# Performance work log

Hardware: AMD Instinct MI355X
Metric: run time of the kernel (lower is better)

Reference implementation:

```python
import jax, jax.numpy as jnp
import numpy as np

N_POINTS = 2_000_000
OUTPUT_DIM = 8
L_RES = 128
H_RES = 1024


def _to_idx(c, size):
    # c in [-1, 1], align_corners=True mapping to pixel coords
    p = (c + 1.0) * 0.5 * (size - 1)
    i0 = jnp.floor(p)
    w = p - i0  # interpolation weight toward i1
    i0 = jnp.clip(i0.astype(jnp.int32), 0, size - 1)
    i1 = jnp.clip(i0 + 1, 0, size - 1)
    return i0, i1, w


def trilinear_sample(grid, coords):
    # grid: [C, D, H, W]; coords: [N, 3] with (x->W, y->H, z->D); returns [C, N]
    C, D, H, W = grid.shape
    x0, x1, wx = _to_idx(coords[:, 0], W)
    y0, y1, wy = _to_idx(coords[:, 1], H)
    z0, z1, wz = _to_idx(coords[:, 2], D)
    g = lambda zi, yi, xi: grid[:, zi, yi, xi]  # gather -> [C, N]
    out = (g(z0, y0, x0) * ((1 - wz) * (1 - wy) * (1 - wx))
           + g(z0, y0, x1) * ((1 - wz) * (1 - wy) * wx)
           + g(z0, y1, x0) * ((1 - wz) * wy * (1 - wx))
           + g(z0, y1, x1) * ((1 - wz) * wy * wx)
           + g(z1, y0, x0) * (wz * (1 - wy) * (1 - wx))
           + g(z1, y0, x1) * (wz * (1 - wy) * wx)
           + g(z1, y1, x0) * (wz * wy * (1 - wx))
           + g(z1, y1, x1) * (wz * wy * wx))
    return out


def bilinear_sample(plane, coords):
    # plane: [C, H, W]; coords: [N, 2] with (x->W, y->H); returns [C, N]
    C, H, W = plane.shape
    x0, x1, wx = _to_idx(coords[:, 0], W)
    y0, y1, wy = _to_idx(coords[:, 1], H)
    g = lambda yi, xi: plane[:, yi, xi]  # [C, N]
    out = (g(y0, x0) * ((1 - wy) * (1 - wx))
           + g(y0, x1) * ((1 - wy) * wx)
           + g(y1, x0) * (wy * (1 - wx))
           + g(y1, x1) * (wy * wx))
    return out


def setup_inputs() -> dict:
    key = jax.random.key(0)
    k1, k2, k3 = jax.random.split(key, 3)
    xyz = jax.random.uniform(k1, (N_POINTS, 3), dtype=jnp.float32)  # in [0,1) subset of [-1,1]
    L_grid = jax.random.normal(k2, (1, OUTPUT_DIM, L_RES, L_RES, L_RES), dtype=jnp.float32) * 0.1
    H_planes = jax.random.normal(k3, (3, OUTPUT_DIM, H_RES, H_RES), dtype=jnp.float32) * 0.1
    return {"xyz": xyz, "bound": 1, "L_grid": L_grid, "H_planes": H_planes}


def reference(xyz, bound, L_grid, H_planes):
    xyz_norm = xyz / bound  # [N, 3]
    L_out = trilinear_sample(L_grid[0], xyz_norm)  # [C, N]
    H_out = (bilinear_sample(H_planes[0], xyz_norm[:, jnp.array([0, 1])])
             + bilinear_sample(H_planes[1], xyz_norm[:, jnp.array([1, 2])])
             + bilinear_sample(H_planes[2], xyz_norm[:, jnp.array([2, 0])]))
    return (L_out + H_out).T  # [N, C]
```

## Files before the change

kernel.cpp:

```cpp
#include <hip/hip_runtime.h>

#define LRES 128
#define HRES 1024
#define NB 256
#define BTS 1024
#define NBUCK 512
#define RCAP 8192

static const int LVOX = LRES * LRES * LRES;
static const int PPIX = HRES * HRES;
static const int TV = LVOX + 3 * PPIX;

typedef float f32x4 __attribute__((ext_vector_type(4)));
typedef unsigned u32x4 __attribute__((ext_vector_type(4)));


__device__ __forceinline__ void to_idx(float c, int size, int& i0, int& i1, float& w) {
    float p = (c + 1.0f) * 0.5f * (float)(size - 1);
    float f = floorf(p);
    w = p - f;
    int i = (int)f;
    i0 = min(max(i, 0), size - 1);
    i1 = min(i0 + 1, size - 1);
}

__device__ __forceinline__ unsigned f2bf(float f) {
    unsigned u = __float_as_uint(f);
    return (u + 0x7FFFu + ((u >> 16) & 1u)) >> 16;
}
__device__ __forceinline__ float bflo(unsigned u) { return __uint_as_float(u << 16); }
__device__ __forceinline__ float bfhi(unsigned u) { return __uint_as_float(u & 0xFFFF0000u); }

__device__ __forceinline__ void fma8u(f32x4& a0, f32x4& a1, uint4 q, float w) {
    a0.x = fmaf(bflo(q.x), w, a0.x);
    a0.y = fmaf(bfhi(q.x), w, a0.y);
    a0.z = fmaf(bflo(q.y), w, a0.z);
    a0.w = fmaf(bfhi(q.y), w, a0.w);
    a1.x = fmaf(bflo(q.z), w, a1.x);
    a1.y = fmaf(bfhi(q.z), w, a1.y);
    a1.z = fmaf(bflo(q.w), w, a1.z);
    a1.w = fmaf(bfhi(q.w), w, a1.w);
}

__device__ __forceinline__ unsigned spread3(unsigned x) {
    x &= 0x3FFu;
    x = (x | (x << 16)) & 0x030000FFu;
    x = (x | (x << 8)) & 0x0300F00Fu;
    x = (x | (x << 4)) & 0x030C30C3u;
    x = (x | (x << 2)) & 0x09249249u;
    return x;
}
__device__ __forceinline__ unsigned morton21(float x, float y, float z) {
    int px = min(max((int)(x * 128.f), 0), 127);
    int py = min(max((int)(y * 128.f), 0), 127);
    int pz = min(max((int)(z * 128.f), 0), 127);
    return spread3(px) | (spread3(py) << 1) | (spread3(pz) << 2);
}

__global__ __launch_bounds__(BTS) void prep_k(const float* __restrict__ xyz,
                                              const int* __restrict__ boundp,
                                              const float* __restrict__ Lg,
                                              const float* __restrict__ Hp,
                                              unsigned* __restrict__ hmat,
                                              u32x4* __restrict__ gclb,
                                              u32x4* __restrict__ pclb, int N) {
    __shared__ unsigned h[NBUCK];
    int b = blockIdx.x;
    if (b < NB) {
        for (int i = threadIdx.x; i < NBUCK; i += BTS) h[i] = 0u;
        __syncthreads();
        float invb = 1.0f / (float)boundp[0];
        for (int n = b * BTS + threadIdx.x; n < N; n += NB * BTS) {
            float x = xyz[(size_t)3 * n + 0] * invb;
            float y = xyz[(size_t)3 * n + 1] * invb;
            float z = xyz[(size_t)3 * n + 2] * invb;
            atomicAdd(&h[morton21(x, y, z) >> 12], 1u);
        }
        __syncthreads();
        for (int i = threadIdx.x; i < NBUCK; i += BTS)
            hmat[(size_t)b * NBUCK + i] = h[i];
    } else {
        int v = ((b - NB) * BTS + threadIdx.x) * 2;
        if (v >= TV) return;
        unsigned ha[8], hb[8];
        u32x4* dst;
        if (v < LVOX) {
#pragma unroll
            for (int c = 0; c < 8; ++c) {
                float2 f = *(const float2*)(Lg + (size_t)c * LVOX + v);
                ha[c] = f2bf(f.x);
                hb[c] = f2bf(f.y);
            }
            dst = gclb + v;
        } else {
            int u = v - LVOX;
            int p = u >> 20;
            int r = u & (PPIX - 1);
            const float* src = Hp + (size_t)p * 8 * PPIX;
#pragma unroll
            for (int c = 0; c < 8; ++c) {
                float2 f = *(const float2*)(src + (size_t)c * PPIX + r);
                ha[c] = f2bf(f.x);
                hb[c] = f2bf(f.y);
            }
            dst = pclb + (size_t)p * PPIX + r;
        }
        u32x4 o1, o2;
        o1.x = ha[0] | (ha[1] << 16); o1.y = ha[2] | (ha[3] << 16);
        o1.z = ha[4] | (ha[5] << 16); o1.w = ha[6] | (ha[7] << 16);
        o2.x = hb[0] | (hb[1] << 16); o2.y = hb[2] | (hb[3] << 16);
        o2.z = hb[4] | (hb[5] << 16); o2.w = hb[6] | (hb[7] << 16);
        __builtin_nontemporal_store(o1, dst);
        __builtin_nontemporal_store(o2, dst + 1);
    }
}

__global__ __launch_bounds__(1024) void offsets_k(unsigned* __restrict__ hmat,
                                                  unsigned* __restrict__ bb) {
    __shared__ unsigned tot[NBUCK];
    __shared__ unsigned cbase[NBUCK];
    int t = threadIdx.x;
    unsigned run = 0;
    if (t < NBUCK) {
        for (int b = 0; b < NB; ++b) {
            unsigned v = hmat[(size_t)b * NBUCK + t];
            hmat[(size_t)b * NBUCK + t] = run;
            run += v;
        }
        tot[t] = run;
    }
    __syncthreads();
    for (int o = 1; o < NBUCK; o <<= 1) {
        unsigned v = 0;
        if (t < NBUCK && t >= o) v = tot[t - o];
        __syncthreads();
        if (t < NBUCK) tot[t] += v;
        __syncthreads();
    }
    if (t < NBUCK) {
        unsigned excl = tot[t] - run;
        cbase[t] = excl;
        bb[t] = excl;
        if (t == NBUCK - 1) bb[NBUCK] = tot[t];
    }
    __syncthreads();
    for (int idx = t; idx < NB * NBUCK; idx += 1024)
        hmat[idx] += cbase[idx & (NBUCK - 1)];
}

__global__ __launch_bounds__(BTS) void scatter_k(const float* __restrict__ xyz,
                                                 const int* __restrict__ boundp,
                                                 const unsigned* __restrict__ hmat,
                                                 float4* __restrict__ s1, int N) {
    __shared__ unsigned cnt[NBUCK];
    int b = blockIdx.x;
    for (int i = threadIdx.x; i < NBUCK; i += BTS)
        cnt[i] = hmat[(size_t)b * NBUCK + i];
    __syncthreads();
    float invb = 1.0f / (float)boundp[0];
    for (int n = b * BTS + threadIdx.x; n < N; n += NB * BTS) {
        float x = xyz[(size_t)3 * n + 0] * invb;
        float y = xyz[(size_t)3 * n + 1] * invb;
        float z = xyz[(size_t)3 * n + 2] * invb;
        unsigned key = morton21(x, y, z) >> 12;
        unsigned d = atomicAdd(&cnt[key], 1u);
        s1[d] = make_float4(x, y, z, __int_as_float(n));
    }
}

__global__ __launch_bounds__(1024) void refine_k(const float4* __restrict__ s1,
                                                 const unsigned* __restrict__ bb,
                                                 float4* __restrict__ s2) {
    __shared__ unsigned hist[4096];
    __shared__ unsigned part[1024];
    int b = blockIdx.x;
    unsigned start = bb[b];
    unsigned cnt = bb[b + 1] - start;
    int t = threadIdx.x;
    if (cnt > RCAP) {
        for (unsigned j = t; j < cnt; j += 1024) s2[start + j] = s1[start + j];
        return;
    }
    for (int i = t; i < 4096; i += 1024) hist[i] = 0u;
    __syncthreads();
    float4 rec[RCAP / 1024];
    unsigned key[RCAP / 1024], tick[RCAP / 1024];
#pragma unroll
    for (int k = 0; k < RCAP / 1024; ++k) {
        unsigned j = t + k * 1024u;
        if (j < cnt) {
            rec[k] = s1[start + j];
            key[k] = morton21(rec[k].x, rec[k].y, rec[k].z) & 4095u;
            tick[k] = atomicAdd(&hist[key[k]], 1u);
        }
    }
    __syncthreads();
    unsigned h4[4];
    unsigned s = 0;
#pragma unroll
    for (int k = 0; k < 4; ++k) {
        h4[k] = hist[t * 4 + k];
        s += h4[k];
    }
    part[t] = s;
    __syncthreads();
    for (int o = 1; o < 1024; o <<= 1) {
        unsigned v = (t >= o) ? part[t - o] : 0u;
        __syncthreads();
        part[t] += v;
        __syncthreads();
    }
    unsigned base = part[t] - s;
#pragma unroll
    for (int k = 0; k < 4; ++k) {
        hist[t * 4 + k] = base;
        base += h4[k];
    }
    __syncthreads();
#pragma unroll
    for (int k = 0; k < RCAP / 1024; ++k) {
        unsigned j = t + k * 1024u;
        if (j < cnt) s2[start + hist[key[k]] + tick[k]] = rec[k];
    }
}

__global__ __launch_bounds__(256) void sample_srt(const float4* __restrict__ sorted,
                                                  const uint4* __restrict__ gclb,
                                                  const uint4* __restrict__ pclb,
                                                  float* __restrict__ out, int N) {
    int i = blockIdx.x * blockDim.x + threadIdx.x;
    if (i >= N) return;
    float4 rec = sorted[i];
    float x = rec.x, y = rec.y, z = rec.z;
    int idx = __float_as_int(rec.w);

    int x0, x1, y0, y1, z0, z1;
    float wx, wy, wz;
    to_idx(x, LRES, x0, x1, wx);
    to_idx(y, LRES, y0, y1, wy);
    to_idx(z, LRES, z0, z1, wz);
    const uint4* b00 = gclb + ((size_t)z0 * LRES + y0) * LRES;
    const uint4* b01 = gclb + ((size_t)z0 * LRES + y1) * LRES;
    const uint4* b10 = gclb + ((size_t)z1 * LRES + y0) * LRES;
    const uint4* b11 = gclb + ((size_t)z1 * LRES + y1) * LRES;
    uint4 g0 = b00[x0], g1 = b00[x1], g2 = b01[x0], g3 = b01[x1];
    uint4 g4 = b10[x0], g5 = b10[x1], g6 = b11[x0], g7 = b11[x1];

    const float cw[3] = {x, y, z};
    const float ch[3] = {y, z, x};
    float pww[3], pwh[3];
    uint4 r[12];
#pragma unroll
    for (int p = 0; p < 3; ++p) {
        int w0, w1, h0, h1;
        to_idx(cw[p], HRES, w0, w1, pww[p]);
        to_idx(ch[p], HRES, h0, h1, pwh[p]);
        const uint4* base = pclb + (size_t)p * PPIX;
        const uint4* r0 = base + (size_t)h0 * HRES;
        const uint4* r1 = base + (size_t)h1 * HRES;
        r[4 * p + 0] = r0[w0];
        r[4 * p + 1] = r0[w1];
        r[4 * p + 2] = r1[w0];
        r[4 * p + 3] = r1[w1];
    }

    f32x4 a0 = (f32x4)0.f;
    f32x4 a1 = (f32x4)0.f;
    {
        float ux = 1.f - wx, uy = 1.f - wy, uz = 1.f - wz;
        fma8u(a0, a1, g0, uz * uy * ux);
        fma8u(a0, a1, g1, uz * uy * wx);
        fma8u(a0, a1, g2, uz * wy * ux);
        fma8u(a0, a1, g3, uz * wy * wx);
        fma8u(a0, a1, g4, wz * uy * ux);
        fma8u(a0, a1, g5, wz * uy * wx);
        fma8u(a0, a1, g6, wz * wy * ux);
        fma8u(a0, a1, g7, wz * wy * wx);
    }
#pragma unroll
    for (int p = 0; p < 3; ++p) {
        float ww = pww[p], wh = pwh[p];
        float uw = 1.f - ww, uh = 1.f - wh;
        fma8u(a0, a1, r[4 * p + 0], uh * uw);
        fma8u(a0, a1, r[4 * p + 1], uh * ww);
        fma8u(a0, a1, r[4 * p + 2], wh * uw);
        fma8u(a0, a1, r[4 * p + 3], wh * ww);
    }

    f32x4* o = (f32x4*)(out + (size_t)idx * 8);
    o[0] = a0;
    o[1] = a1;
}

__global__ __launch_bounds__(256) void sample_cf(
    const float* __restrict__ xyz, const int* __restrict__ boundp,
    const float* __restrict__ Lg, const float* __restrict__ Hp,
    float* __restrict__ out, int N) {
    int n = blockIdx.x * blockDim.x + threadIdx.x;
    if (n >= N) return;
    float invb = 1.0f / (float)boundp[0];
    float x = xyz[(size_t)3 * n + 0] * invb;
    float y = xyz[(size_t)3 * n + 1] * invb;
    float z = xyz[(size_t)3 * n + 2] * invb;
    float acc[8];
#pragma unroll
    for (int c = 0; c < 8; ++c) acc[c] = 0.f;
    {
        int x0, x1, y0, y1, z0, z1;
        float wx, wy, wz;
        to_idx(x, LRES, x0, x1, wx);
        to_idx(y, LRES, y0, y1, wy);
        to_idx(z, LRES, z0, z1, wz);
        float ux = 1.f - wx, uy = 1.f - wy, uz = 1.f - wz;
        size_t i8[8];
        i8[0] = ((size_t)z0 * LRES + y0) * LRES + x0;
        i8[1] = ((size_t)z0 * LRES + y0) * LRES + x1;
        i8[2] = ((size_t)z0 * LRES + y1) * LRES + x0;
        i8[3] = ((size_t)z0 * LRES + y1) * LRES + x1;
        i8[4] = ((size_t)z1 * LRES + y0) * LRES + x0;
        i8[5] = ((size_t)z1 * LRES + y0) * LRES + x1;
        i8[6] = ((size_t)z1 * LRES + y1) * LRES + x0;
        i8[7] = ((size_t)z1 * LRES + y1) * LRES + x1;
        float w8[8] = {uz * uy * ux, uz * uy * wx, uz * wy * ux, uz * wy * wx,
                       wz * uy * ux, wz * uy * wx, wz * wy * ux, wz * wy * wx};
#pragma unroll
        for (int c = 0; c < 8; ++c) {
            const float* g = Lg + (size_t)c * LVOX;
            float s = 0.f;
#pragma unroll
            for (int k = 0; k < 8; ++k) s = fmaf(g[i8[k]], w8[k], s);
            acc[c] += s;
        }
    }
    {
        const float cw[3] = {x, y, z};
        const float ch[3] = {y, z, x};
        for (int p = 0; p < 3; ++p) {
            int w0, w1, h0, h1;
            float ww, wh;
            to_idx(cw[p], HRES, w0, w1, ww);
            to_idx(ch[p], HRES, h0, h1, wh);
            float uw = 1.f - ww, uh = 1.f - wh;
            size_t i4[4] = {(size_t)h0 * HRES + w0, (size_t)h0 * HRES + w1,
                            (size_t)h1 * HRES + w0, (size_t)h1 * HRES + w1};
            float w4[4] = {uh * uw, uh * ww, wh * uw, wh * ww};
            const float* pb = Hp + (size_t)p * 8 * PPIX;
#pragma unroll
            for (int c = 0; c < 8; ++c) {
                const float* g = pb + (size_t)c * PPIX;
                float s = 0.f;
#pragma unroll
                for (int k = 0; k < 4; ++k) s = fmaf(g[i4[k]], w4[k], s);
                acc[c] += s;
            }
        }
    }
#pragma unroll
    for (int c = 0; c < 8; ++c) out[(size_t)n * 8 + c] = acc[c];
}

extern "C" void kernel_launch(void* const* d_in, const int* in_sizes, int n_in,
                              void* d_out, int out_size, void* d_ws, size_t ws_size,
                              hipStream_t stream) {
    const float* xyz = (const float*)d_in[0];
    const int* bound = (const int*)d_in[1];
    const float* Lg = (const float*)d_in[2];
    const float* Hp = (const float*)d_in[3];
    float* out = (float*)d_out;
    int N = in_sizes[0] / 3;

    size_t off = 0;
    size_t gclb_b = (size_t)LVOX * 16;
    size_t pclb_b = (size_t)3 * PPIX * 16;
    size_t s1_b = (size_t)N * 16;
    size_t s2_b = (size_t)N * 16;
    size_t hmat_b = (size_t)NB * NBUCK * 4;
    size_t bb_b = (size_t)(NBUCK + 1) * 4;
    size_t need = gclb_b + pclb_b + s1_b + s2_b + hmat_b + bb_b;

    if (ws_size >= need) {
        char* w = (char*)d_ws;
        u32x4* gclb = (u32x4*)(w + off);       off += gclb_b;
        u32x4* pclb = (u32x4*)(w + off);       off += pclb_b;
        float4* s1 = (float4*)(w + off);       off += s1_b;
        float4* s2 = (float4*)(w + off);       off += s2_b;
        unsigned* hmat = (unsigned*)(w + off); off += hmat_b;
        unsigned* bb = (unsigned*)(w + off);

        int prep_blocks = NB + (TV / 2 + BTS - 1) / BTS;
        prep_k<<<prep_blocks, BTS, 0, stream>>>(xyz, bound, Lg, Hp, hmat, gclb, pclb, N);
        offsets_k<<<1, 1024, 0, stream>>>(hmat, bb);
        scatter_k<<<NB, BTS, 0, stream>>>(xyz, bound, hmat, s1, N);
        refine_k<<<NBUCK, 1024, 0, stream>>>(s1, bb, s2);
        sample_srt<<<(N + 255) / 256, 256, 0, stream>>>(s2, (const uint4*)gclb,
                                                        (const uint4*)pclb, out, N);
    } else {
        sample_cf<<<(N + 255) / 256, 256, 0, stream>>>(xyz, bound, Lg, Hp, out, N);
    }
}
```

Measured before the change: 408.3 us.

## Vectorize xyz loads, widen grid conversion, and transpose histogram matrix layout

The histogram and scatter kernels now read xyz as three 16-byte vectors covering four points per thread, instead of three scalar loads per point. The bf16 grid conversion handles four voxels per thread with 16-byte nontemporal loads, halving the number of conversion blocks. The per-block histogram matrix is transposed to bucket-major order, so the prefix-scan thread for each bucket walks a contiguous row with vector loads and the base-offset pass is vectorized. The aim is fewer memory transactions in the preprocessing kernels. In exchange each thread holds more registers, and the scatter order inside a bucket changes.

Measured after the change: 497.7 us. +21.9%, slower.

```diff
diff --git a/kernel.cpp b/kernel.cpp
--- a/kernel.cpp
+++ b/kernel.cpp
@@ -70,48 +70,58 @@
         for (int i = threadIdx.x; i < NBUCK; i += BTS) h[i] = 0u;
         __syncthreads();
         float invb = 1.0f / (float)boundp[0];
-        for (int n = b * BTS + threadIdx.x; n < N; n += NB * BTS) {
-            float x = xyz[(size_t)3 * n + 0] * invb;
-            float y = xyz[(size_t)3 * n + 1] * invb;
-            float z = xyz[(size_t)3 * n + 2] * invb;
-            atomicAdd(&h[morton21(x, y, z) >> 12], 1u);
+        int NG = (N + 3) >> 2;
+        for (int g = b * BTS + threadIdx.x; g < NG; g += NB * BTS) {
+            int n0 = g << 2;
+            if (n0 + 4 <= N) {
+                f32x4 qa = *(const f32x4*)(xyz + (size_t)n0 * 3);
+                f32x4 qb = *(const f32x4*)(xyz + (size_t)n0 * 3 + 4);
+                f32x4 qc = *(const f32x4*)(xyz + (size_t)n0 * 3 + 8);
+                atomicAdd(&h[morton21(qa.x * invb, qa.y * invb, qa.z * invb) >> 12], 1u);
+                atomicAdd(&h[morton21(qa.w * invb, qb.x * invb, qb.y * invb) >> 12], 1u);
+                atomicAdd(&h[morton21(qb.z * invb, qb.w * invb, qc.x * invb) >> 12], 1u);
+                atomicAdd(&h[morton21(qc.y * invb, qc.z * invb, qc.w * invb) >> 12], 1u);
+            } else {
+                for (int n = n0; n < N; ++n) {
+                    float x = xyz[(size_t)3 * n + 0] * invb;
+                    float y = xyz[(size_t)3 * n + 1] * invb;
+                    float z = xyz[(size_t)3 * n + 2] * invb;
+                    atomicAdd(&h[morton21(x, y, z) >> 12], 1u);
+                }
+            }
         }
         __syncthreads();
         for (int i = threadIdx.x; i < NBUCK; i += BTS)
-            hmat[(size_t)b * NBUCK + i] = h[i];
+            hmat[(size_t)i * NB + b] = h[i];
     } else {
-        int v = ((b - NB) * BTS + threadIdx.x) * 2;
+        int v = ((b - NB) * BTS + threadIdx.x) * 4;
         if (v >= TV) return;
-        unsigned ha[8], hb[8];
+        f32x4 f[8];
         u32x4* dst;
         if (v < LVOX) {
 #pragma unroll
-            for (int c = 0; c < 8; ++c) {
-                float2 f = *(const float2*)(Lg + (size_t)c * LVOX + v);
-                ha[c] = f2bf(f.x);
-                hb[c] = f2bf(f.y);
-            }
+            for (int c = 0; c < 8; ++c)
+                f[c] = __builtin_nontemporal_load((const f32x4*)(Lg + (size_t)c * LVOX + v));
             dst = gclb + v;
         } else {
             int u = v - LVOX;
             int p = u >> 20;
             int r = u & (PPIX - 1);
-            const float* src = Hp + (size_t)p * 8 * PPIX;
-#pragma unroll
-            for (int c = 0; c < 8; ++c) {
-                float2 f = *(const float2*)(src + (size_t)c * PPIX + r);
-                ha[c] = f2bf(f.x);
-                hb[c] = f2bf(f.y);
-            }
+            const float* src = Hp + (size_t)p * 8 * PPIX + r;
+#pragma unroll
+            for (int c = 0; c < 8; ++c)
+                f[c] = __builtin_nontemporal_load((const f32x4*)(src + (size_t)c * PPIX));
             dst = pclb + (size_t)p * PPIX + r;
         }
-        u32x4 o1, o2;
-        o1.x = ha[0] | (ha[1] << 16); o1.y = ha[2] | (ha[3] << 16);
-        o1.z = ha[4] | (ha[5] << 16); o1.w = ha[6] | (ha[7] << 16);
-        o2.x = hb[0] | (hb[1] << 16); o2.y = hb[2] | (hb[3] << 16);
-        o2.z = hb[4] | (hb[5] << 16); o2.w = hb[6] | (hb[7] << 16);
-        __builtin_nontemporal_store(o1, dst);
-        __builtin_nontemporal_store(o2, dst + 1);
+#pragma unroll
+        for (int e = 0; e < 4; ++e) {
+            u32x4 o;
+            o.x = f2bf(f[0][e]) | (f2bf(f[1][e]) << 16);
+            o.y = f2bf(f[2][e]) | (f2bf(f[3][e]) << 16);
+            o.z = f2bf(f[4][e]) | (f2bf(f[5][e]) << 16);
+            o.w = f2bf(f[6][e]) | (f2bf(f[7][e]) << 16);
+            __builtin_nontemporal_store(o, dst + e);
+        }
     }
 }
 
@@ -122,10 +132,20 @@
     int t = threadIdx.x;
     unsigned run = 0;
     if (t < NBUCK) {
-        for (int b = 0; b < NB; ++b) {
-            unsigned v = hmat[(size_t)b * NBUCK + t];
-            hmat[(size_t)b * NBUCK + t] = run;
-            run += v;
+        u32x4* row = (u32x4*)(hmat + (size_t)t * NB);
+        for (int ch = 0; ch < NB / 32; ++ch) {
+            u32x4 q[8];
+#pragma unroll
+            for (int k = 0; k < 8; ++k) q[k] = row[ch * 8 + k];
+#pragma unroll
+            for (int k = 0; k < 8; ++k) {
+                unsigned v0 = q[k].x, v1 = q[k].y, v2 = q[k].z, v3 = q[k].w;
+                q[k].x = run; run += v0;
+                q[k].y = run; run += v1;
+                q[k].z = run; run += v2;
+                q[k].w = run; run += v3;
+                row[ch * 8 + k] = q[k];
+            }
         }
         tot[t] = run;
     }
@@ -144,8 +164,13 @@
         if (t == NBUCK - 1) bb[NBUCK] = tot[t];
     }
     __syncthreads();
-    for (int idx = t; idx < NB * NBUCK; idx += 1024)
-        hmat[idx] += cbase[idx & (NBUCK - 1)];
+    u32x4* hm4 = (u32x4*)hmat;
+    for (int idx = t; idx < NB * NBUCK / 4; idx += 1024) {
+        u32x4 q = hm4[idx];
+        unsigned cb = cbase[idx >> 6];
+        q.x += cb; q.y += cb; q.z += cb; q.w += cb;
+        hm4[idx] = q;
+    }
 }
 
 __global__ __launch_bounds__(BTS) void scatter_k(const float* __restrict__ xyz,
@@ -155,16 +180,45 @@
     __shared__ unsigned cnt[NBUCK];
     int b = blockIdx.x;
     for (int i = threadIdx.x; i < NBUCK; i += BTS)
-        cnt[i] = hmat[(size_t)b * NBUCK + i];
+        cnt[i] = hmat[(size_t)i * NB + b];
     __syncthreads();
     float invb = 1.0f / (float)boundp[0];
-    for (int n = b * BTS + threadIdx.x; n < N; n += NB * BTS) {
-        float x = xyz[(size_t)3 * n + 0] * invb;
-        float y = xyz[(size_t)3 * n + 1] * invb;
-        float z = xyz[(size_t)3 * n + 2] * invb;
-        unsigned key = morton21(x, y, z) >> 12;
-        unsigned d = atomicAdd(&cnt[key], 1u);
-        s1[d] = make_float4(x, y, z, __int_as_float(n));
+    int NG = (N + 3) >> 2;
+    for (int g = b * BTS + threadIdx.x; g < NG; g += NB * BTS) {
+        int n0 = g << 2;
+        if (n0 + 4 <= N) {
+            f32x4 qa = *(const f32x4*)(xyz + (size_t)n0 * 3);
+            f32x4 qb = *(const f32x4*)(xyz + (size_t)n0 * 3 + 4);
+            f32x4 qc = *(const f32x4*)(xyz + (size_t)n0 * 3 + 8);
+            {
+                float x = qa.x * invb, y = qa.y * invb, z = qa.z * invb;
+                unsigned d = atomicAdd(&cnt[morton21(x, y, z) >> 12], 1u);
+                s1[d] = make_float4(x, y, z, __int_as_float(n0 + 0));
+            }
+            {
+                float x = qa.w * invb, y = qb.x * invb, z = qb.y * invb;
+                unsigned d = atomicAdd(&cnt[morton21(x, y, z) >> 12], 1u);
+                s1[d] = make_float4(x, y, z, __int_as_float(n0 + 1));
+            }
+            {
+                float x = qb.z * invb, y = qb.w * invb, z = qc.x * invb;
+                unsigned d = atomicAdd(&cnt[morton21(x, y, z) >> 12], 1u);
+                s1[d] = make_float4(x, y, z, __int_as_float(n0 + 2));
+            }
+            {
+                float x = qc.y * invb, y = qc.z * invb, z = qc.w * invb;
+                unsigned d = atomicAdd(&cnt[morton21(x, y, z) >> 12], 1u);
+                s1[d] = make_float4(x, y, z, __int_as_float(n0 + 3));
+            }
+        } else {
+            for (int n = n0; n < N; ++n) {
+                float x = xyz[(size_t)3 * n + 0] * invb;
+                float y = xyz[(size_t)3 * n + 1] * invb;
+                float z = xyz[(size_t)3 * n + 2] * invb;
+                unsigned d = atomicAdd(&cnt[morton21(x, y, z) >> 12], 1u);
+                s1[d] = make_float4(x, y, z, __int_as_float(n));
+            }
+        }
     }
 }
 
@@ -387,7 +441,7 @@
         unsigned* hmat = (unsigned*)(w + off); off += hmat_b;
         unsigned* bb = (unsigned*)(w + off);
 
-        int prep_blocks = NB + (TV / 2 + BTS - 1) / BTS;
+        int prep_blocks = NB + (TV / 4 + BTS - 1) / BTS;
         prep_k<<<prep_blocks, BTS, 0, stream>>>(xyz, bound, Lg, Hp, hmat, gclb, pclb, N);
         offsets_k<<<1, 1024, 0, stream>>>(hmat, bb);
         scatter_k<<<NB, BTS, 0, stream>>>(xyz, bound, hmat, s1, N);
```
